# Kernel optimization log

Measured on AMD Instinct MI355X. Metric: run time of the kernel, lower is better.

The kernel has to match this reference:

```python
import jax, jax.numpy as jnp
import numpy as np

BATCH, SEQ, H_IN, N_STATE, H_OUT = 16, 4096, 128, 256, 128
RMIN, RMAX, MAX_PHASE = 0.9, 1.0, 6.283


def setup_inputs() -> dict:
    key = jax.random.key(0)
    ks = jax.random.split(key, 9)
    u = jax.random.normal(ks[0], (BATCH, SEQ, H_IN), jnp.float32)
    # LRU exponential parameterization init (matches torch __init__)
    u1 = jax.random.uniform(ks[1], (N_STATE,), jnp.float32)
    u2 = jax.random.uniform(ks[2], (N_STATE,), jnp.float32)
    nu_log = jnp.log(-0.5 * jnp.log(u1 * (RMAX + RMIN) * (RMAX - RMIN) + RMIN ** 2))
    theta_log = jnp.log(MAX_PHASE * u2)
    lam_abs = jnp.exp(-jnp.exp(nu_log))
    gamma_log = jnp.log(jnp.sqrt(1.0 - lam_abs ** 2))
    s2in = np.sqrt(2.0 * H_IN).astype(np.float32)
    B_re = jax.random.normal(ks[3], (N_STATE, H_IN), jnp.float32) / s2in
    B_im = jax.random.normal(ks[4], (N_STATE, H_IN), jnp.float32) / s2in
    sst = np.sqrt(float(N_STATE)).astype(np.float32)
    C_re = jax.random.normal(ks[5], (H_OUT, N_STATE), jnp.float32) / sst
    C_im = jax.random.normal(ks[6], (H_OUT, N_STATE), jnp.float32) / sst
    D = jax.random.normal(ks[7], (H_OUT, H_IN), jnp.float32) / np.sqrt(float(H_IN)).astype(np.float32)
    return dict(u=u, nu_log=nu_log, theta_log=theta_log, gamma_log=gamma_log,
                B_re=B_re, B_im=B_im, C_re=C_re, C_im=C_im, D=D)


def _combine(a, b):
    # complex affine composition: (l, x) o (l', x') -> (l*l', l'*x + x')
    l1r, l1i, x1r, x1i = a
    l2r, l2i, x2r, x2i = b
    lr = l1r * l2r - l1i * l2i
    li = l1r * l2i + l1i * l2r
    xr = l2r * x1r - l2i * x1i + x2r
    xi = l2r * x1i + l2i * x1r + x2i
    return (lr, li, xr, xi)


def reference(u, nu_log, theta_log, gamma_log, B_re, B_im, C_re, C_im, D):
    lam_mod = jnp.exp(-jnp.exp(nu_log))          # |lambda|, [N]
    th = jnp.exp(theta_log)
    lam_re = lam_mod * jnp.cos(th)
    lam_im = lam_mod * jnp.sin(th)
    gammas = jnp.exp(gamma_log)                  # [N]
    # input projection Bu_t = gamma * (B @ u_t), complex -> real/imag parts
    Bu_re = jnp.einsum('blh,nh->bln', u, B_re) * gammas  # [B,L,N]
    Bu_im = jnp.einsum('blh,nh->bln', u, B_im) * gammas
    Bsz, L, N = Bu_re.shape
    lr = jnp.broadcast_to(lam_re, (Bsz, L, N))
    li = jnp.broadcast_to(lam_im, (Bsz, L, N))
    # parallel scan of x_t = lambda * x_{t-1} + Bu_t, x0 = 0
    _, _, xr, xi = jax.lax.associative_scan(_combine, (lr, li, Bu_re, Bu_im), axis=1)
    zero = jnp.zeros((Bsz, 1, N), u.dtype)
    pre_re = jnp.concatenate([zero, xr[:, :-1]], axis=1)  # states[:, :-1]
    pre_im = jnp.concatenate([zero, xi[:, :-1]], axis=1)
    # y_t = Re(C x_{t-1}) + D u_t
    y = (jnp.einsum('bln,on->blo', pre_re, C_re)
         - jnp.einsum('bln,on->blo', pre_im, C_im)
         + jnp.einsum('blh,oh->blo', u, D))
    return y
```

## Files before the change

kernel.cpp:

```cpp
#include <hip/hip_runtime.h>
#include <math.h>

#define BATCH 16
#define SEQ   4096
#define HIN   128
#define NST   256
#define HOUT  128
#define CL    32
#define NC    (SEQ/CL)
#define ROWS  (BATCH*SEQ)
#define KTOT  640
#define NBU   512

typedef __attribute__((ext_vector_type(8))) short short8;
typedef __attribute__((ext_vector_type(4))) float f32x4;

__device__ inline unsigned short f2bf(float f) {
  union { float f; unsigned u; } v; v.f = f;
  unsigned r = v.u + 0x7FFFu + ((v.u >> 16) & 1u);
  return (unsigned short)(r >> 16);
}
__device__ inline float bf2f(unsigned short s) {
  union { unsigned u; float f; } v; v.u = ((unsigned)s) << 16;
  return v.f;
}

__global__ __launch_bounds__(256) void k_prep(
    const float* __restrict__ nu_log, const float* __restrict__ theta_log,
    const float* __restrict__ gamma_log,
    const float* __restrict__ Bre, const float* __restrict__ Bim,
    const float* __restrict__ Cre, const float* __restrict__ Cim,
    const float* __restrict__ Dm,
    float* __restrict__ lamre, float* __restrict__ lamim,
    unsigned short* __restrict__ Wb, unsigned short* __restrict__ W) {
  int idx = blockIdx.x*256 + threadIdx.x;
  if (idx < NST) {
    float lm = expf(-expf(nu_log[idx]));
    float th = expf(theta_log[idx]);
    lamre[idx] = lm * cosf(th);
    lamim[idx] = lm * sinf(th);
  }
  if (idx < 512*HIN) {
    int r = idx >> 7, h = idx & 127;
    int g = r >> 7;
    int w = r & 127;
    int n = g*64 + (w & 63);
    float gm = expf(gamma_log[n]);
    float v = (w < 64) ? Bre[n*HIN + h] : Bim[n*HIN + h];
    Wb[idx] = f2bf(gm * v);
  }
  if (idx < HOUT*KTOT) {
    int o = idx / KTOT, k = idx - o*KTOT;
    float v;
    if (k < NST)        v =  Cre[o*NST + k];
    else if (k < 2*NST) v = -Cim[o*NST + (k - NST)];
    else                v =  Dm[o*HIN + (k - 2*NST)];
    W[idx] = f2bf(v);
  }
}

__global__ __launch_bounds__(256) void k_cast(
    const float* __restrict__ u, unsigned short* __restrict__ ubf) {
  size_t i = (size_t)(blockIdx.x*256 + threadIdx.x) * 4;
  float4 v = *(const float4*)(u + i);
  ushort4 o;
  o.x = f2bf(v.x); o.y = f2bf(v.y); o.z = f2bf(v.z); o.w = f2bf(v.w);
  *(ushort4*)(ubf + i) = o;
}

union SharedU {
  struct { unsigned short A[128][72], B[128][72]; } s1;
  struct { float stg[2][32][132]; } s2;
};
__global__ __launch_bounds__(256) void k_bu(
    const unsigned short* __restrict__ ubf, const unsigned short* __restrict__ Wb,
    const float* __restrict__ lamre, const float* __restrict__ lamim,
    unsigned short* __restrict__ bu16,
    float* __restrict__ S_re, float* __restrict__ S_im) {
  __shared__ SharedU sh;
  int tid = threadIdx.x;
  int row0 = blockIdx.x * 128;
  int g    = blockIdx.y;
  int col0 = g * 128;
  int wid = tid >> 6, lane = tid & 63;
  int lm = lane & 15, lq = lane >> 4;
  int m0 = (wid >> 1) * 64, n0 = (wid & 1) * 64;
  f32x4 acc[4][4];
#pragma unroll
  for (int i = 0; i < 4; ++i)
#pragma unroll
    for (int j = 0; j < 4; ++j) acc[i][j] = (f32x4)0.f;
  for (int s = 0; s < 2; ++s) {
#pragma unroll
    for (int cc = 0; cc < 4; ++cc) {
      int ch = cc*256 + tid;
      int r = ch >> 3, h0 = (ch & 7) * 8;
      *(short8*)&sh.s1.A[r][h0] = *(const short8*)&ubf[(size_t)(row0 + r)*HIN + s*64 + h0];
      *(short8*)&sh.s1.B[r][h0] = *(const short8*)&Wb [(size_t)(col0 + r)*HIN + s*64 + h0];
    }
    __syncthreads();
#pragma unroll
    for (int ks = 0; ks < 2; ++ks) {
      int k0 = ks*32 + lq*8;
      short8 a[4], b[4];
#pragma unroll
      for (int i = 0; i < 4; ++i) a[i] = *(const short8*)&sh.s1.A[m0 + i*16 + lm][k0];
#pragma unroll
      for (int j = 0; j < 4; ++j) b[j] = *(const short8*)&sh.s1.B[n0 + j*16 + lm][k0];
#pragma unroll
      for (int i = 0; i < 4; ++i)
#pragma unroll
        for (int j = 0; j < 4; ++j)
          acc[i][j] = __builtin_amdgcn_mfma_f32_16x16x32_bf16(a[i], b[j], acc[i][j], 0, 0, 0);
    }
    __syncthreads();
  }
#pragma unroll
  for (int i = 0; i < 4; ++i)
#pragma unroll
    for (int j = 0; j < 4; ++j)
#pragma unroll
      for (int r = 0; r < 4; ++r)
        bu16[(size_t)(row0 + m0 + i*16 + lq*4 + r)*NBU + col0 + n0 + j*16 + lm] =
            f2bf(acc[i][j][r]);
  int b = row0 >> 12;
  int cbase = (row0 & 4095) >> 5;
  for (int p = 0; p < 2; ++p) {
    __syncthreads();
#pragma unroll
    for (int ii = 0; ii < 2; ++ii) {
      int i = 2*p + ii;
#pragma unroll
      for (int j = 0; j < 4; ++j)
#pragma unroll
        for (int r = 0; r < 4; ++r) {
          int trow = ii*16 + lq*4 + r;
          sh.s2.stg[wid >> 1][trow][n0 + j*16 + lm] = acc[i][j][r];
        }
    }
    __syncthreads();
    if (tid < 128) {
      int buf = tid >> 6, n = tid & 63;
      int ng = g*64 + n;
      float lr = lamre[ng], li = lamim[ng];
      float sr = 0.f, si = 0.f;
#pragma unroll
      for (int t = 0; t < 32; ++t) {
        float br = sh.s2.stg[buf][t][n];
        float bi = sh.s2.stg[buf][t][64 + n];
        float nr = lr*sr - li*si + br;
        float ni = lr*si + li*sr + bi;
        sr = nr; si = ni;
      }
      int c = cbase + p + 2*buf;
      int idx = (b*NC + c)*NST + ng;
      S_re[idx] = sr; S_im[idx] = si;
    }
  }
}

__global__ __launch_bounds__(256) void k_carry2(
    const float* __restrict__ S_re, const float* __restrict__ S_im,
    const float* __restrict__ lamre, const float* __restrict__ lamim,
    float* __restrict__ G_re, float* __restrict__ G_im) {
  int blk = blockIdx.x;
  int b = blk >> 3, g = blk & 7;
  int n = threadIdx.x;
  float ar = lamre[n], ai = lamim[n];
#pragma unroll
  for (int s = 0; s < 5; ++s) { float nr = ar*ar - ai*ai, ni = 2.f*ar*ai; ar = nr; ai = ni; }
  float tr = 0.f, ti = 0.f;
#pragma unroll
  for (int cc = 0; cc < 16; ++cc) {
    int idx = (b*NC + g*16 + cc)*NST + n;
    float nr = ar*tr - ai*ti + S_re[idx];
    float ni = ar*ti + ai*tr + S_im[idx];
    tr = nr; ti = ni;
  }
  int gi = (b*8 + g)*NST + n;
  G_re[gi] = tr; G_im[gi] = ti;
}

__global__ __launch_bounds__(256) void k_final(
    const float* __restrict__ S_re, const float* __restrict__ S_im,
    const float* __restrict__ G_re, const float* __restrict__ G_im,
    const float* __restrict__ lamre, const float* __restrict__ lamim,
    float* __restrict__ X0_re, float* __restrict__ X0_im) {
  int blk = blockIdx.x;
  int b = blk >> 3, g = blk & 7;
  int n = threadIdx.x;
  float ar = lamre[n], ai = lamim[n];
#pragma unroll
  for (int s = 0; s < 5; ++s) { float nr = ar*ar - ai*ai, ni = 2.f*ar*ai; ar = nr; ai = ni; }
  float a5r = ar, a5i = ai;
#pragma unroll
  for (int s = 0; s < 4; ++s) { float nr = a5r*a5r - a5i*a5i, ni = 2.f*a5r*a5i; a5r = nr; a5i = ni; }
  float pr = 0.f, pi = 0.f;
  for (int j = 0; j < g; ++j) {
    int gi = (b*8 + j)*NST + n;
    float nr = a5r*pr - a5i*pi + G_re[gi];
    float ni = a5r*pi + a5i*pr + G_im[gi];
    pr = nr; pi = ni;
  }
  float xr = pr, xi = pi;
#pragma unroll
  for (int cc = 0; cc < 16; ++cc) {
    int idx = (b*NC + g*16 + cc)*NST + n;
    X0_re[idx] = xr; X0_im[idx] = xi;
    float nr = ar*xr - ai*xi + S_re[idx];
    float ni = ar*xi + ai*xr + S_im[idx];
    xr = nr; xi = ni;
  }
}

__global__ __launch_bounds__(256) void k_scan(
    const unsigned short* __restrict__ bu16, const unsigned short* __restrict__ ubf,
    const float* __restrict__ X0_re, const float* __restrict__ X0_im,
    const float* __restrict__ lamre, const float* __restrict__ lamim,
    unsigned short* __restrict__ pre16) {
  int blk = blockIdx.x;
  int b = blk >> 7, c = blk & (NC-1);
  int tid = threadIdx.x;
  int t0 = c*CL;
  size_t rowbase = (size_t)(b*SEQ + t0);
  {
    const unsigned short* usrc = ubf + rowbase*HIN;
    unsigned short* udst = pre16 + rowbase*KTOT + 2*NST;
#pragma unroll
    for (int c2 = tid; c2 < 512; c2 += 256) {
      int t = c2 >> 4, h0 = (c2 & 15) * 8;
      *(short8*)&udst[(size_t)t*KTOT + h0] = *(const short8*)&usrc[t*HIN + h0];
    }
  }
  int n = tid;
  int gg = n >> 6, nl = n & 63;
  int cre = gg*128 + nl, cim = cre + 64;
  const unsigned short* bup = bu16 + rowbase*NBU;
  unsigned short rbr[CL], rbi[CL];
#pragma unroll
  for (int t = 0; t < CL; ++t) {
    rbr[t] = bup[(size_t)t*NBU + cre];
    rbi[t] = bup[(size_t)t*NBU + cim];
  }
  float lr = lamre[n], li = lamim[n];
  int idx = (b*NC + c)*NST + n;
  float xr = X0_re[idx], xi = X0_im[idx];
  unsigned short* pdst = pre16 + rowbase*KTOT;
#pragma unroll
  for (int t = 0; t < CL; ++t) {
    pdst[n]       = f2bf(xr);
    pdst[NST + n] = f2bf(xi);
    float br = bf2f(rbr[t]);
    float bi = bf2f(rbi[t]);
    float nr = lr*xr - li*xi + br;
    float ni = lr*xi + li*xr + bi;
    xr = nr; xi = ni; pdst += KTOT;
  }
}

#define OP 8
__global__ __launch_bounds__(256) void k_out2(
    const unsigned short* __restrict__ pre16, const unsigned short* __restrict__ W,
    float* __restrict__ y) {
  __shared__ unsigned short Asl[128][128+OP];
  __shared__ unsigned short Bsl[128][128+OP];
  int tid = threadIdx.x;
  int row0 = blockIdx.x * 128;
  int wid = tid >> 6, lane = tid & 63;
  int lm = lane & 15, lq = lane >> 4;
  int m0 = (wid >> 1) * 64, n0 = (wid & 1) * 64;
  f32x4 acc[4][4];
#pragma unroll
  for (int i = 0; i < 4; ++i)
#pragma unroll
    for (int j = 0; j < 4; ++j) acc[i][j] = (f32x4)0.f;
  for (int s = 0; s < 5; ++s) {
#pragma unroll
    for (int cc = 0; cc < 8; ++cc) {
      int ch = cc*256 + tid;
      int r = ch >> 4, h0 = (ch & 15) * 8;
      *(short8*)&Asl[r][h0] = *(const short8*)&pre16[(size_t)(row0 + r)*KTOT + s*128 + h0];
      *(short8*)&Bsl[r][h0] = *(const short8*)&W[(size_t)r*KTOT + s*128 + h0];
    }
    __syncthreads();
#pragma unroll
    for (int ks = 0; ks < 4; ++ks) {
      int k0 = ks*32 + lq*8;
      short8 a[4], b[4];
#pragma unroll
      for (int i = 0; i < 4; ++i) a[i] = *(const short8*)&Asl[m0 + i*16 + lm][k0];
#pragma unroll
      for (int j = 0; j < 4; ++j) b[j] = *(const short8*)&Bsl[n0 + j*16 + lm][k0];
#pragma unroll
      for (int i = 0; i < 4; ++i)
#pragma unroll
        for (int j = 0; j < 4; ++j)
          acc[i][j] = __builtin_amdgcn_mfma_f32_16x16x32_bf16(a[i], b[j], acc[i][j], 0, 0, 0);
    }
    __syncthreads();
  }
#pragma unroll
  for (int i = 0; i < 4; ++i)
#pragma unroll
    for (int j = 0; j < 4; ++j)
#pragma unroll
      for (int r = 0; r < 4; ++r)
        y[(size_t)(row0 + m0 + i*16 + lq*4 + r)*HOUT + n0 + j*16 + lm] = acc[i][j][r];
}

extern "C" void kernel_launch(void* const* d_in, const int* in_sizes, int n_in,
                              void* d_out, int out_size, void* d_ws, size_t ws_size,
                              hipStream_t stream) {
  const float* u         = (const float*)d_in[0];
  const float* nu_log    = (const float*)d_in[1];
  const float* theta_log = (const float*)d_in[2];
  const float* gamma_log = (const float*)d_in[3];
  const float* B_re      = (const float*)d_in[4];
  const float* B_im      = (const float*)d_in[5];
  const float* C_re      = (const float*)d_in[6];
  const float* C_im      = (const float*)d_in[7];
  const float* Dm        = (const float*)d_in[8];
  float* y = (float*)d_out;
  char* ws = (char*)d_ws;

  float*          lamre = (float*)(ws);
  float*          lamim = (float*)(ws + 1024);
  unsigned short* ubf   = (unsigned short*)(ws + 4096);
  unsigned short* Wb    = (unsigned short*)(ws + 4096 + 16777216);
  unsigned short* W     = (unsigned short*)(ws + 4096 + 16777216 + 131072);
  unsigned short* bu16  = (unsigned short*)(ws + 4096 + 16777216 + 131072 + 163840);
  char* pp = ws + 4096 + 16777216 + 131072 + 163840 + (size_t)ROWS*NBU*2;
  unsigned short* pre16 = (unsigned short*)pp;
  char* p2 = pp + (size_t)ROWS*KTOT*2;
  float* S_re  = (float*)(p2);
  float* S_im  = (float*)(p2 + 2097152);
  float* G_re  = (float*)(p2 + 2*2097152);
  float* G_im  = (float*)(p2 + 2*2097152 + 131072);
  float* X0_re = (float*)(p2 + 2*2097152 + 2*131072);
  float* X0_im = (float*)(p2 + 3*2097152 + 2*131072);

  k_prep<<<320, 256, 0, stream>>>(nu_log, theta_log, gamma_log, B_re, B_im,
                                  C_re, C_im, Dm, lamre, lamim, Wb, W);
  k_cast<<<(ROWS*HIN)/1024, 256, 0, stream>>>(u, ubf);
  k_bu<<<dim3(ROWS/128, 4), 256, 0, stream>>>(ubf, Wb, lamre, lamim,
                                              bu16, S_re, S_im);
  k_carry2<<<BATCH*8, 256, 0, stream>>>(S_re, S_im, lamre, lamim, G_re, G_im);
  k_final<<<BATCH*8, 256, 0, stream>>>(S_re, S_im, G_re, G_im, lamre, lamim,
                                       X0_re, X0_im);
  k_scan<<<BATCH*NC, 256, 0, stream>>>(bu16, ubf, X0_re, X0_im, lamre, lamim, pre16);
  k_out2<<<ROWS/128, 256, 0, stream>>>(pre16, W, y);
}
```

Baseline: 189.4 us.

## Stop copying u into pre16; read ubf directly in output GEMM and restructure k_bu

The scan kernel no longer copies the bf16 input rows into the pre16 buffer. pre16 is narrowed to 512 columns, and the output GEMM reads its last K slice straight from ubf, which removes a redundant write and read of the input. k_bu now loads the A tile once and loops over all four column groups inside one block instead of launching a 4-wide grid. This cuts repeated loads of A but gives four times fewer blocks, so there is less parallelism per launch.

Result: no change. 187.9 us (-0.8%).

```diff
diff --git a/kernel.cpp b/kernel.cpp
--- a/kernel.cpp
+++ b/kernel.cpp
@@ -10,6 +10,7 @@
 #define NC    (SEQ/CL)
 #define ROWS  (BATCH*SEQ)
 #define KTOT  640
+#define NPRE  512
 #define NBU   512
 
 typedef __attribute__((ext_vector_type(8))) short short8;
@@ -68,93 +69,97 @@
   *(ushort4*)(ubf + i) = o;
 }
 
-union SharedU {
-  struct { unsigned short A[128][72], B[128][72]; } s1;
-  struct { float stg[2][32][132]; } s2;
+union SharedBu {
+  unsigned short B[128][136];
+  float stg[2][32][132];
 };
 __global__ __launch_bounds__(256) void k_bu(
     const unsigned short* __restrict__ ubf, const unsigned short* __restrict__ Wb,
     const float* __restrict__ lamre, const float* __restrict__ lamim,
     unsigned short* __restrict__ bu16,
     float* __restrict__ S_re, float* __restrict__ S_im) {
-  __shared__ SharedU sh;
+  __shared__ unsigned short Asl[128][136];
+  __shared__ SharedBu sh;
   int tid = threadIdx.x;
   int row0 = blockIdx.x * 128;
-  int g    = blockIdx.y;
-  int col0 = g * 128;
   int wid = tid >> 6, lane = tid & 63;
   int lm = lane & 15, lq = lane >> 4;
   int m0 = (wid >> 1) * 64, n0 = (wid & 1) * 64;
-  f32x4 acc[4][4];
-#pragma unroll
-  for (int i = 0; i < 4; ++i)
-#pragma unroll
-    for (int j = 0; j < 4; ++j) acc[i][j] = (f32x4)0.f;
-  for (int s = 0; s < 2; ++s) {
-#pragma unroll
-    for (int cc = 0; cc < 4; ++cc) {
-      int ch = cc*256 + tid;
-      int r = ch >> 3, h0 = (ch & 7) * 8;
-      *(short8*)&sh.s1.A[r][h0] = *(const short8*)&ubf[(size_t)(row0 + r)*HIN + s*64 + h0];
-      *(short8*)&sh.s1.B[r][h0] = *(const short8*)&Wb [(size_t)(col0 + r)*HIN + s*64 + h0];
-    }
-    __syncthreads();
-#pragma unroll
-    for (int ks = 0; ks < 2; ++ks) {
-      int k0 = ks*32 + lq*8;
-      short8 a[4], b[4];
-#pragma unroll
-      for (int i = 0; i < 4; ++i) a[i] = *(const short8*)&sh.s1.A[m0 + i*16 + lm][k0];
-#pragma unroll
-      for (int j = 0; j < 4; ++j) b[j] = *(const short8*)&sh.s1.B[n0 + j*16 + lm][k0];
-#pragma unroll
-      for (int i = 0; i < 4; ++i)
-#pragma unroll
-        for (int j = 0; j < 4; ++j)
-          acc[i][j] = __builtin_amdgcn_mfma_f32_16x16x32_bf16(a[i], b[j], acc[i][j], 0, 0, 0);
-    }
-    __syncthreads();
-  }
-#pragma unroll
-  for (int i = 0; i < 4; ++i)
-#pragma unroll
-    for (int j = 0; j < 4; ++j)
-#pragma unroll
-      for (int r = 0; r < 4; ++r)
-        bu16[(size_t)(row0 + m0 + i*16 + lq*4 + r)*NBU + col0 + n0 + j*16 + lm] =
-            f2bf(acc[i][j][r]);
   int b = row0 >> 12;
   int cbase = (row0 & 4095) >> 5;
-  for (int p = 0; p < 2; ++p) {
+#pragma unroll
+  for (int cc = 0; cc < 8; ++cc) {
+    int ch = cc*256 + tid;
+    int r = ch >> 4, h0 = (ch & 15) * 8;
+    *(short8*)&Asl[r][h0] = *(const short8*)&ubf[(size_t)(row0 + r)*HIN + h0];
+  }
+  for (int g = 0; g < 4; ++g) {
     __syncthreads();
 #pragma unroll
-    for (int ii = 0; ii < 2; ++ii) {
-      int i = 2*p + ii;
+    for (int cc = 0; cc < 8; ++cc) {
+      int ch = cc*256 + tid;
+      int r = ch >> 4, h0 = (ch & 15) * 8;
+      *(short8*)&sh.B[r][h0] = *(const short8*)&Wb[(size_t)(g*128 + r)*HIN + h0];
+    }
+    __syncthreads();
+    f32x4 acc[4][4];
+#pragma unroll
+    for (int i = 0; i < 4; ++i)
+#pragma unroll
+      for (int j = 0; j < 4; ++j) acc[i][j] = (f32x4)0.f;
+#pragma unroll
+    for (int ks = 0; ks < 4; ++ks) {
+      int k0 = ks*32 + lq*8;
+      short8 a[4], bb[4];
+#pragma unroll
+      for (int i = 0; i < 4; ++i) a[i] = *(const short8*)&Asl[m0 + i*16 + lm][k0];
+#pragma unroll
+      for (int j = 0; j < 4; ++j) bb[j] = *(const short8*)&sh.B[n0 + j*16 + lm][k0];
+#pragma unroll
+      for (int i = 0; i < 4; ++i)
+#pragma unroll
+        for (int j = 0; j < 4; ++j)
+          acc[i][j] = __builtin_amdgcn_mfma_f32_16x16x32_bf16(a[i], bb[j], acc[i][j], 0, 0, 0);
+    }
+#pragma unroll
+    for (int i = 0; i < 4; ++i)
 #pragma unroll
       for (int j = 0; j < 4; ++j)
 #pragma unroll
-        for (int r = 0; r < 4; ++r) {
-          int trow = ii*16 + lq*4 + r;
-          sh.s2.stg[wid >> 1][trow][n0 + j*16 + lm] = acc[i][j][r];
+        for (int r = 0; r < 4; ++r)
+          bu16[(size_t)(row0 + m0 + i*16 + lq*4 + r)*NBU + g*128 + n0 + j*16 + lm] =
+              f2bf(acc[i][j][r]);
+    for (int p = 0; p < 2; ++p) {
+      __syncthreads();
+#pragma unroll
+      for (int ii = 0; ii < 2; ++ii) {
+        int i = 2*p + ii;
+#pragma unroll
+        for (int j = 0; j < 4; ++j)
+#pragma unroll
+          for (int r = 0; r < 4; ++r) {
+            int trow = ii*16 + lq*4 + r;
+            sh.stg[wid >> 1][trow][n0 + j*16 + lm] = acc[i][j][r];
+          }
+      }
+      __syncthreads();
+      if (tid < 128) {
+        int buf = tid >> 6, nl = tid & 63;
+        int ng = g*64 + nl;
+        float lr = lamre[ng], li = lamim[ng];
+        float sr = 0.f, si = 0.f;
+#pragma unroll
+        for (int t = 0; t < 32; ++t) {
+          float br = sh.stg[buf][t][nl];
+          float bi = sh.stg[buf][t][64 + nl];
+          float nr = lr*sr - li*si + br;
+          float ni = lr*si + li*sr + bi;
+          sr = nr; si = ni;
         }
-    }
-    __syncthreads();
-    if (tid < 128) {
-      int buf = tid >> 6, n = tid & 63;
-      int ng = g*64 + n;
-      float lr = lamre[ng], li = lamim[ng];
-      float sr = 0.f, si = 0.f;
-#pragma unroll
-      for (int t = 0; t < 32; ++t) {
-        float br = sh.s2.stg[buf][t][n];
-        float bi = sh.s2.stg[buf][t][64 + n];
-        float nr = lr*sr - li*si + br;
-        float ni = lr*si + li*sr + bi;
-        sr = nr; si = ni;
+        int c = cbase + buf*2 + p;
+        int idx = (b*NC + c)*NST + ng;
+        S_re[idx] = sr; S_im[idx] = si;
       }
-      int c = cbase + p + 2*buf;
-      int idx = (b*NC + c)*NST + ng;
-      S_re[idx] = sr; S_im[idx] = si;
     }
   }
 }
@@ -214,7 +219,7 @@
 }
 
 __global__ __launch_bounds__(256) void k_scan(
-    const unsigned short* __restrict__ bu16, const unsigned short* __restrict__ ubf,
+    const unsigned short* __restrict__ bu16,
     const float* __restrict__ X0_re, const float* __restrict__ X0_im,
     const float* __restrict__ lamre, const float* __restrict__ lamim,
     unsigned short* __restrict__ pre16) {
@@ -223,15 +228,6 @@
   int tid = threadIdx.x;
   int t0 = c*CL;
   size_t rowbase = (size_t)(b*SEQ + t0);
-  {
-    const unsigned short* usrc = ubf + rowbase*HIN;
-    unsigned short* udst = pre16 + rowbase*KTOT + 2*NST;
-#pragma unroll
-    for (int c2 = tid; c2 < 512; c2 += 256) {
-      int t = c2 >> 4, h0 = (c2 & 15) * 8;
-      *(short8*)&udst[(size_t)t*KTOT + h0] = *(const short8*)&usrc[t*HIN + h0];
-    }
-  }
   int n = tid;
   int gg = n >> 6, nl = n & 63;
   int cre = gg*128 + nl, cim = cre + 64;
@@ -245,7 +241,7 @@
   float lr = lamre[n], li = lamim[n];
   int idx = (b*NC + c)*NST + n;
   float xr = X0_re[idx], xi = X0_im[idx];
-  unsigned short* pdst = pre16 + rowbase*KTOT;
+  unsigned short* pdst = pre16 + rowbase*NPRE;
 #pragma unroll
   for (int t = 0; t < CL; ++t) {
     pdst[n]       = f2bf(xr);
@@ -254,16 +250,15 @@
     float bi = bf2f(rbi[t]);
     float nr = lr*xr - li*xi + br;
     float ni = lr*xi + li*xr + bi;
-    xr = nr; xi = ni; pdst += KTOT;
-  }
-}
-
-#define OP 8
+    xr = nr; xi = ni; pdst += NPRE;
+  }
+}
+
 __global__ __launch_bounds__(256) void k_out2(
-    const unsigned short* __restrict__ pre16, const unsigned short* __restrict__ W,
-    float* __restrict__ y) {
-  __shared__ unsigned short Asl[128][128+OP];
-  __shared__ unsigned short Bsl[128][128+OP];
+    const unsigned short* __restrict__ pre16, const unsigned short* __restrict__ ubf,
+    const unsigned short* __restrict__ W, float* __restrict__ y) {
+  __shared__ unsigned short Asl[128][136];
+  __shared__ unsigned short Bsl[128][136];
   int tid = threadIdx.x;
   int row0 = blockIdx.x * 128;
   int wid = tid >> 6, lane = tid & 63;
@@ -279,23 +274,26 @@
     for (int cc = 0; cc < 8; ++cc) {
       int ch = cc*256 + tid;
       int r = ch >> 4, h0 = (ch & 15) * 8;
-      *(short8*)&Asl[r][h0] = *(const short8*)&pre16[(size_t)(row0 + r)*KTOT + s*128 + h0];
+      if (s < 4)
+        *(short8*)&Asl[r][h0] = *(const short8*)&pre16[(size_t)(row0 + r)*NPRE + s*128 + h0];
+      else
+        *(short8*)&Asl[r][h0] = *(const short8*)&ubf[(size_t)(row0 + r)*HIN + h0];
       *(short8*)&Bsl[r][h0] = *(const short8*)&W[(size_t)r*KTOT + s*128 + h0];
     }
     __syncthreads();
 #pragma unroll
     for (int ks = 0; ks < 4; ++ks) {
       int k0 = ks*32 + lq*8;
-      short8 a[4], b[4];
+      short8 a[4], bb[4];
 #pragma unroll
       for (int i = 0; i < 4; ++i) a[i] = *(const short8*)&Asl[m0 + i*16 + lm][k0];
 #pragma unroll
-      for (int j = 0; j < 4; ++j) b[j] = *(const short8*)&Bsl[n0 + j*16 + lm][k0];
+      for (int j = 0; j < 4; ++j) bb[j] = *(const short8*)&Bsl[n0 + j*16 + lm][k0];
 #pragma unroll
       for (int i = 0; i < 4; ++i)
 #pragma unroll
         for (int j = 0; j < 4; ++j)
-          acc[i][j] = __builtin_amdgcn_mfma_f32_16x16x32_bf16(a[i], b[j], acc[i][j], 0, 0, 0);
+          acc[i][j] = __builtin_amdgcn_mfma_f32_16x16x32_bf16(a[i], bb[j], acc[i][j], 0, 0, 0);
     }
     __syncthreads();
   }
@@ -331,7 +329,7 @@
   unsigned short* bu16  = (unsigned short*)(ws + 4096 + 16777216 + 131072 + 163840);
   char* pp = ws + 4096 + 16777216 + 131072 + 163840 + (size_t)ROWS*NBU*2;
   unsigned short* pre16 = (unsigned short*)pp;
-  char* p2 = pp + (size_t)ROWS*KTOT*2;
+  char* p2 = pp + (size_t)ROWS*NPRE*2;
   float* S_re  = (float*)(p2);
   float* S_im  = (float*)(p2 + 2097152);
   float* G_re  = (float*)(p2 + 2*2097152);
@@ -342,11 +340,10 @@
   k_prep<<<320, 256, 0, stream>>>(nu_log, theta_log, gamma_log, B_re, B_im,
                                   C_re, C_im, Dm, lamre, lamim, Wb, W);
   k_cast<<<(ROWS*HIN)/1024, 256, 0, stream>>>(u, ubf);
-  k_bu<<<dim3(ROWS/128, 4), 256, 0, stream>>>(ubf, Wb, lamre, lamim,
-                                              bu16, S_re, S_im);
+  k_bu<<<ROWS/128, 256, 0, stream>>>(ubf, Wb, lamre, lamim, bu16, S_re, S_im);
   k_carry2<<<BATCH*8, 256, 0, stream>>>(S_re, S_im, lamre, lamim, G_re, G_im);
   k_final<<<BATCH*8, 256, 0, stream>>>(S_re, S_im, G_re, G_im, lamre, lamim,
                                        X0_re, X0_im);
-  k_scan<<<BATCH*NC, 256, 0, stream>>>(bu16, ubf, X0_re, X0_im, lamre, lamim, pre16);
-  k_out2<<<ROWS/128, 256, 0, stream>>>(pre16, W, y);
-}
+  k_scan<<<BATCH*NC, 256, 0, stream>>>(bu16, X0_re, X0_im, lamre, lamim, pre16);
+  k_out2<<<ROWS/128, 256, 0, stream>>>(pre16, ubf, W, y);
+}
```
